# Kernel tuning notes

Measured on AMD Instinct MI355X. Metric: run time of the kernel, lower is better.

## Reference

```python
import jax, jax.numpy as jnp
import numpy as np

N_NODES = 8192
EMBED = 64
N_NEURONS = [512, 256, 128]
ACTION_SIZE = 8
BATCH = 4096


def setup_inputs() -> dict:
    key = jax.random.key(0)
    ks = jax.random.split(key, 16)
    in_size = 2 * N_NODES + 2 * EMBED

    def u(k, shape, bound):
        return jax.random.uniform(k, shape, jnp.float32, -bound, bound)

    stdv1 = 1.0 / np.sqrt(N_NEURONS[0])
    stdv2 = 1.0 / np.sqrt(EMBED)
    return {
        "state": jax.random.uniform(ks[0], (N_NODES, N_NODES), jnp.float32),
        "start": jax.random.randint(ks[1], (BATCH,), 0, N_NODES),
        "end": jax.random.randint(ks[2], (BATCH,), 0, N_NODES),
        # GCN layer params
        "gw1": u(ks[3], (1, N_NEURONS[0]), stdv1),
        "gb1": u(ks[4], (N_NEURONS[0],), stdv1),
        "gw2": u(ks[5], (N_NEURONS[0], EMBED), stdv2),
        "gb2": u(ks[6], (EMBED,), stdv2),
        # dense head params (xavier-ish)
        "fw1": u(ks[7], (in_size, N_NEURONS[0]), np.sqrt(6.0 / (in_size + N_NEURONS[0]))),
        "fb1": jnp.zeros((N_NEURONS[0],), jnp.float32),
        "fw2": u(ks[8], (N_NEURONS[0], N_NEURONS[1]), np.sqrt(6.0 / (N_NEURONS[0] + N_NEURONS[1]))),
        "fb2": jnp.zeros((N_NEURONS[1],), jnp.float32),
        "fw3": u(ks[9], (N_NEURONS[1], N_NEURONS[2]), np.sqrt(6.0 / (N_NEURONS[1] + N_NEURONS[2]))),
        "fb3": jnp.zeros((N_NEURONS[2],), jnp.float32),
        "fw4": u(ks[10], (N_NEURONS[2], ACTION_SIZE), np.sqrt(6.0 / (N_NEURONS[2] + ACTION_SIZE))),
        "fb4": jnp.zeros((ACTION_SIZE,), jnp.float32),
    }


def reference(state, start, end, gw1, gb1, gw2, gb2,
              fw1, fb1, fw2, fb2, fw3, fb3, fw4, fb4):
    # x = diag(state) as [N, 1] node features
    x = jnp.diagonal(state)[:, None]
    # adj = state with zeroed diagonal, detached (no grad through adj)
    adj = jax.lax.stop_gradient(jnp.fill_diagonal(state, 0.0, inplace=False))
    # GCN layer 1: relu(adj @ (x @ W) + b); dropout is identity in eval mode
    h = jax.nn.relu(adj @ (x @ gw1) + gb1)              # [N, 512]
    # GCN layer 2
    h = jax.nn.relu(adj @ (h @ gw2) + gb2)              # [N, 64]
    h = jax.nn.log_softmax(h, axis=1)                   # [N, 64]
    # gather node features and embeddings for each (start, end) edge
    edge_features = jnp.concatenate(
        [state[start], state[end], h[start], h[end]], axis=1)  # [B, 2N+2E]
    y = jax.nn.relu(edge_features @ fw1 + fb1)
    y = jax.nn.relu(y @ fw2 + fb2)                      # d1 dropout: identity (eval)
    y = jax.nn.relu(y @ fw3 + fb3)
    action_q = jax.nn.relu(y @ fw4 + fb4)               # [B, action_size]
    return action_q
```

## Files before the change

### kernel.cpp

```cpp
#include <hip/hip_runtime.h>
#include <hip/hip_bf16.h>
#include <math.h>

#define NN 8192
#define EMB 64
#define H1D 512
#define NB 4096

typedef __bf16 bf16x8 __attribute__((ext_vector_type(8)));
typedef float f32x4 __attribute__((ext_vector_type(4)));
typedef unsigned short u16x8 __attribute__((ext_vector_type(8)));
typedef unsigned short u16x4 __attribute__((ext_vector_type(4)));

__device__ __forceinline__ unsigned short f2bf(float f) {
    return __bfloat16_as_ushort(__float2bfloat16(f));
}

__device__ __forceinline__ void gload16(const void* g, void* l) {
    __builtin_amdgcn_global_load_lds(
        (const __attribute__((address_space(1))) void*)g,
        (__attribute__((address_space(3))) void*)l, 16, 0, 0);
}

__global__ void k_diag(const float* __restrict__ state, float* __restrict__ diag) {
    int i = blockIdx.x * blockDim.x + threadIdx.x;
    if (i < NN) diag[i] = state[(size_t)i * NN + i];
}

__global__ __launch_bounds__(256) void k_convert(const float* __restrict__ state,
                                                 const float* __restrict__ diag,
                                                 unsigned short* __restrict__ stateb,
                                                 float* __restrict__ s) {
    int row = blockIdx.x;
    int tid = threadIdx.x;
    const float4* st4 = (const float4*)(state + (size_t)row * NN);
    const float4* dg4 = (const float4*)diag;
    unsigned short* drow = stateb + (size_t)row * NN;
    float acc = 0.f;
#pragma unroll
    for (int t = 0; t < 8; ++t) {
        int f = t * 256 + tid;
        float4 a = st4[f], d = dg4[f];
        acc += a.x * d.x + a.y * d.y + a.z * d.z + a.w * d.w;
        u16x4 o;
        o[0] = f2bf(a.x); o[1] = f2bf(a.y); o[2] = f2bf(a.z); o[3] = f2bf(a.w);
        *(u16x4*)&drow[f * 4] = o;
    }
#pragma unroll
    for (int m = 32; m >= 1; m >>= 1) acc += __shfl_xor(acc, m);
    __shared__ float red[4];
    if ((tid & 63) == 0) red[tid >> 6] = acc;
    __syncthreads();
    if (tid == 0) {
        float tot = red[0] + red[1] + red[2] + red[3];
        float d = diag[row];
        s[row] = tot - d * d;
    }
}

__global__ __launch_bounds__(256) void k_tr_fw1(const float* __restrict__ fw1,
                                                unsigned short* __restrict__ fw1t) {
    __shared__ float t[64][65];
    int kb = blockIdx.x * 64, nb = blockIdx.y * 64;
    int tid = threadIdx.x;
#pragma unroll
    for (int i = 0; i < 4; ++i) {
        int lin = i * 256 + tid;
        int r = lin >> 4, c4 = (lin & 15) << 2;
        float4 v = *(const float4*)&fw1[(size_t)(kb + r) * 512 + nb + c4];
        t[r][c4] = v.x; t[r][c4 + 1] = v.y; t[r][c4 + 2] = v.z; t[r][c4 + 3] = v.w;
    }
    __syncthreads();
#pragma unroll
    for (int i = 0; i < 4; ++i) {
        int lin = i * 256 + tid;
        int n = lin >> 4, k4 = (lin & 15) << 2;
        u16x4 o;
        o[0] = f2bf(t[k4 + 0][n]); o[1] = f2bf(t[k4 + 1][n]);
        o[2] = f2bf(t[k4 + 2][n]); o[3] = f2bf(t[k4 + 3][n]);
        *(u16x4*)&fw1t[(size_t)(nb + n) * 16512 + kb + k4] = o;
    }
}

__global__ __launch_bounds__(256) void k_tr_q(const float* __restrict__ q,
                                              unsigned short* __restrict__ qbT) {
    __shared__ float t[64][65];
    int kb = blockIdx.x * 64;
    int tid = threadIdx.x;
#pragma unroll
    for (int i = 0; i < 4; ++i) {
        int lin = i * 256 + tid;
        int r = lin >> 4, c4 = (lin & 15) << 2;
        float4 v = *(const float4*)&q[(size_t)(kb + r) * 64 + c4];
        t[r][c4] = v.x; t[r][c4 + 1] = v.y; t[r][c4 + 2] = v.z; t[r][c4 + 3] = v.w;
    }
    __syncthreads();
#pragma unroll
    for (int i = 0; i < 4; ++i) {
        int lin = i * 256 + tid;
        int c = lin >> 4, k4 = (lin & 15) << 2;
        u16x4 o;
        o[0] = f2bf(t[k4 + 0][c]); o[1] = f2bf(t[k4 + 1][c]);
        o[2] = f2bf(t[k4 + 2][c]); o[3] = f2bf(t[k4 + 3][c]);
        *(u16x4*)&qbT[(size_t)c * 8192 + kb + k4] = o;
    }
}

__global__ __launch_bounds__(256) void k_rowdot(const float* __restrict__ state,
                                                const float* __restrict__ diag,
                                                float* __restrict__ s) {
    int row = blockIdx.x;
    int tid = threadIdx.x;
    const float4* st4 = (const float4*)(state + (size_t)row * NN);
    const float4* dg4 = (const float4*)diag;
    float acc = 0.f;
#pragma unroll
    for (int t = 0; t < 8; ++t) {
        int f = t * 256 + tid;
        float4 a = st4[f], d = dg4[f];
        acc += a.x * d.x + a.y * d.y + a.z * d.z + a.w * d.w;
    }
#pragma unroll
    for (int m = 32; m >= 1; m >>= 1) acc += __shfl_xor(acc, m);
    __shared__ float red[4];
    if ((tid & 63) == 0) red[tid >> 6] = acc;
    __syncthreads();
    if (tid == 0) {
        float tot = red[0] + red[1] + red[2] + red[3];
        float d = diag[row];
        s[row] = tot - d * d;
    }
}

__global__ __launch_bounds__(256) void k_q(const float* __restrict__ s,
                                           const float* __restrict__ gw1,
                                           const float* __restrict__ gb1,
                                           const float* __restrict__ gw2,
                                           float* __restrict__ q) {
    int tid = threadIdx.x;
    int c = tid & 63;
    int row = blockIdx.x * 4 + (tid >> 6);
    float sv = s[row];
    float acc = 0.f;
    for (int j = 0; j < H1D; ++j) {
        float hv = fmaxf(fmaf(sv, gw1[j], gb1[j]), 0.f);
        acc = fmaf(hv, gw2[j * EMB + c], acc);
    }
    q[row * EMB + c] = acc;
}


__global__ __launch_bounds__(256) void k_gcn2_mfma_b(const unsigned short* __restrict__ stateb,
                                                     const unsigned short* __restrict__ qbT,
                                                     float* __restrict__ partg) {
    __shared__ __align__(16) unsigned short Asm[2][64 * 64];
    __shared__ __align__(16) unsigned short Bsm[2][64 * 64];
    const int tid = threadIdx.x;
    const int l = tid & 63, wv = tid >> 6;
    const int rbase = blockIdx.x * 64;
    const int kbase0 = blockIdx.y * 1024;

    const unsigned short* aP[2]; const unsigned short* bP[2]; int lb[2];
#pragma unroll
    for (int i = 0; i < 2; ++i) {
        int slot = i * 256 + tid;
        int r = slot >> 3, cg = slot & 7;
        aP[i] = stateb + (size_t)(rbase + r) * NN + kbase0 + ((cg ^ (r & 7)) << 3);
        bP[i] = qbT + (size_t)r * 8192 + kbase0 + ((cg ^ (r & 7)) << 3);
        lb[i] = (i * 256 + wv * 64) * 8;
    }

    f32x4 acc[4] = {};
    const int fr = l & 15, fq = l >> 4;

#pragma unroll
    for (int i = 0; i < 2; ++i) {
        gload16(aP[i], &Asm[0][lb[i]]);
        gload16(bP[i], &Bsm[0][lb[i]]);
    }
    __syncthreads();

    int buf = 0;
    for (int kt = 0; kt < 16; ++kt) {
        if (kt < 15) {
#pragma unroll
            for (int i = 0; i < 2; ++i) {
                gload16(aP[i] + (kt + 1) * 64, &Asm[buf ^ 1][lb[i]]);
                gload16(bP[i] + (kt + 1) * 64, &Bsm[buf ^ 1][lb[i]]);
            }
        }
#pragma unroll
        for (int kh = 0; kh < 2; ++kh) {
            int ch = kh * 4 + fq;
            int row = wv * 16 + fr;
            bf16x8 aF = *(const bf16x8*)&Asm[buf][row * 64 + ((ch ^ (row & 7)) << 3)];
            bf16x8 bF[4];
#pragma unroll
            for (int n = 0; n < 4; ++n) {
                int col = n * 16 + fr;
                bF[n] = *(const bf16x8*)&Bsm[buf][col * 64 + ((ch ^ (col & 7)) << 3)];
            }
#pragma unroll
            for (int n = 0; n < 4; ++n)
                acc[n] = __builtin_amdgcn_mfma_f32_16x16x32_bf16(aF, bF[n], acc[n], 0, 0, 0);
        }
        __syncthreads();
        buf ^= 1;
    }

    float* dst = partg + (size_t)blockIdx.y * (NN * EMB);
#pragma unroll
    for (int n = 0; n < 4; ++n) {
        int row0 = rbase + wv * 16 + fq * 4;
        int col = n * 16 + fr;
#pragma unroll
        for (int j = 0; j < 4; ++j)
            dst[(size_t)(row0 + j) * EMB + col] = acc[n][j];
    }
}

__global__ __launch_bounds__(256) void k_gcn2_combine_b(const float* __restrict__ partg,
                                                        const float* __restrict__ diag,
                                                        const float* __restrict__ q,
                                                        const float* __restrict__ gb2,
                                                        unsigned short* __restrict__ hb) {
    int tid = threadIdx.x;
    int c = tid & 63;
    int row = blockIdx.x * 4 + (tid >> 6);
    int idx = row * EMB + c;
    float v = gb2[c] - diag[row] * q[idx];
#pragma unroll
    for (int p = 0; p < 8; ++p) v += partg[(size_t)p * NN * EMB + idx];
    v = fmaxf(v, 0.f);
    float mx = v;
#pragma unroll
    for (int m = 32; m >= 1; m >>= 1) mx = fmaxf(mx, __shfl_xor(mx, m));
    float e = expf(v - mx);
    float sum = e;
#pragma unroll
    for (int m = 32; m >= 1; m >>= 1) sum += __shfl_xor(sum, m);
    hb[idx] = f2bf(v - mx - logf(sum));
}

__global__ __launch_bounds__(256) void k_head1_mfma_b(
    const unsigned short* __restrict__ stateb, const unsigned short* __restrict__ hb,
    const int* __restrict__ start, const int* __restrict__ end,
    const unsigned short* __restrict__ fw1t, float* __restrict__ parth) {
    __shared__ __align__(16) unsigned short Asm[2][64 * 64];
    __shared__ __align__(16) unsigned short Bsm[2][128 * 64];
    __shared__ int ridx[64];
    const int tid = threadIdx.x;
    const int l = tid & 63, wv = tid >> 6;
    const int rbase = blockIdx.x * 64, cbase = blockIdx.y * 128;
    const int ks = blockIdx.z, side = ks >> 1, half = ks & 1;
    if (tid < 64) ridx[tid] = (side ? end : start)[rbase + tid];
    __syncthreads();

    const unsigned short* aS[2]; const unsigned short* aH[2]; int alb[2];
#pragma unroll
    for (int i = 0; i < 2; ++i) {
        int slot = i * 256 + tid;
        int r = slot >> 3, cg = slot & 7;
        int swz = (cg ^ (r & 7)) << 3;
        int gi = ridx[r];
        aS[i] = stateb + (size_t)gi * NN + half * 4096 + swz;
        aH[i] = hb + gi * EMB + swz;
        alb[i] = (i * 256 + wv * 64) * 8;
    }
    const unsigned short* bP[4]; int blb[4];
#pragma unroll
    for (int i = 0; i < 4; ++i) {
        int slot = i * 256 + tid;
        int n = slot >> 3, cg = slot & 7;
        bP[i] = fw1t + (size_t)(cbase + n) * 16512 + ((cg ^ (n & 7)) << 3);
        blb[i] = (i * 256 + wv * 64) * 8;
    }
    const int kB0 = side * 8192 + half * 4096;
    const int kBtail = 16384 + side * 64;
    const int nsteps = 64 + half;

#pragma unroll
    for (int i = 0; i < 2; ++i) gload16(aS[i], &Asm[0][alb[i]]);
#pragma unroll
    for (int i = 0; i < 4; ++i) gload16(bP[i] + kB0, &Bsm[0][blb[i]]);
    __syncthreads();

    f32x4 acc[2][4] = {};
    const int wm = wv >> 1, wn = wv & 1;
    const int fr = l & 15, fq = l >> 4;

    int buf = 0;
    for (int kt = 0; kt < nsteps; ++kt) {
        int nxt = kt + 1;
        if (nxt < nsteps) {
            if (nxt < 64) {
#pragma unroll
                for (int i = 0; i < 2; ++i) gload16(aS[i] + nxt * 64, &Asm[buf ^ 1][alb[i]]);
#pragma unroll
                for (int i = 0; i < 4; ++i) gload16(bP[i] + kB0 + nxt * 64, &Bsm[buf ^ 1][blb[i]]);
            } else {
#pragma unroll
                for (int i = 0; i < 2; ++i) gload16(aH[i], &Asm[buf ^ 1][alb[i]]);
#pragma unroll
                for (int i = 0; i < 4; ++i) gload16(bP[i] + kBtail, &Bsm[buf ^ 1][blb[i]]);
            }
        }
#pragma unroll
        for (int kh = 0; kh < 2; ++kh) {
            int ch = kh * 4 + fq;
            bf16x8 aF[2], bF[4];
#pragma unroll
            for (int m = 0; m < 2; ++m) {
                int row = wm * 32 + m * 16 + fr;
                aF[m] = *(const bf16x8*)&Asm[buf][row * 64 + ((ch ^ (row & 7)) << 3)];
            }
#pragma unroll
            for (int n = 0; n < 4; ++n) {
                int nl = wn * 64 + n * 16 + fr;
                bF[n] = *(const bf16x8*)&Bsm[buf][nl * 64 + ((ch ^ (nl & 7)) << 3)];
            }
#pragma unroll
            for (int m = 0; m < 2; ++m)
#pragma unroll
                for (int n = 0; n < 4; ++n)
                    acc[m][n] = __builtin_amdgcn_mfma_f32_16x16x32_bf16(
                        aF[m], bF[n], acc[m][n], 0, 0, 0);
        }
        __syncthreads();
        buf ^= 1;
    }

    float* dst = parth + (size_t)ks * (NB * H1D);
#pragma unroll
    for (int m = 0; m < 2; ++m) {
        int row0 = rbase + wm * 32 + m * 16 + fq * 4;
#pragma unroll
        for (int n = 0; n < 4; ++n) {
            int col = cbase + wn * 64 + n * 16 + fr;
#pragma unroll
            for (int j = 0; j < 4; ++j)
                dst[(size_t)(row0 + j) * H1D + col] = acc[m][n][j];
        }
    }
}

__global__ void k_head1_fin4(const float* __restrict__ parth, const float* __restrict__ fb1,
                             float* __restrict__ y1) {
    int i = blockIdx.x * blockDim.x + threadIdx.x;
    const size_t S = (size_t)NB * H1D;
    float4 a = *(const float4*)&parth[(size_t)i * 4];
    float4 b = *(const float4*)&parth[S + (size_t)i * 4];
    float4 c = *(const float4*)&parth[2 * S + (size_t)i * 4];
    float4 d = *(const float4*)&parth[3 * S + (size_t)i * 4];
    float4 bias = *(const float4*)&fb1[(i * 4) & 511];
    float4 o;
    o.x = fmaxf(a.x + b.x + c.x + d.x + bias.x, 0.f);
    o.y = fmaxf(a.y + b.y + c.y + d.y + bias.y, 0.f);
    o.z = fmaxf(a.z + b.z + c.z + d.z + bias.z, 0.f);
    o.w = fmaxf(a.w + b.w + c.w + d.w + bias.w, 0.f);
    *(float4*)&y1[(size_t)i * 4] = o;
}


__global__ __launch_bounds__(256) void k_gcn2_mfma(const float* __restrict__ state,
                                                   const unsigned short* __restrict__ qbT,
                                                   float* __restrict__ partg) {
    __shared__ __align__(16) unsigned short Asm[2][64 * 64];
    __shared__ __align__(16) unsigned short Bsm[2][64 * 64];
    const int tid = threadIdx.x;
    const int l = tid & 63, wv = tid >> 6;
    const int rbase = blockIdx.x * 64;
    const int kbase0 = blockIdx.y * 1024;

    const float* aptr[2]; int awr[2];
#pragma unroll
    for (int i = 0; i < 2; ++i) {
        int slot = i * 256 + tid;
        int r = slot >> 3, cg = slot & 7;
        aptr[i] = state + (size_t)(rbase + r) * NN + kbase0 + cg * 8;
        awr[i] = r * 64 + ((cg ^ (r & 7)) << 3);
    }
    const unsigned short* bptr[2]; int bbase[2];
#pragma unroll
    for (int i = 0; i < 2; ++i) {
        int c = i * 32 + wv * 8 + (l >> 3);
        int cg = l & 7;
        bptr[i] = qbT + (size_t)c * 8192 + kbase0 + ((cg ^ (c & 7)) << 3);
        bbase[i] = i * 2048 + wv * 512;
    }

    f32x4 acc[4] = {};
    const int fr = l & 15, fq = l >> 4;
    float4 va[2][2];

#pragma unroll
    for (int i = 0; i < 2; ++i) {
        va[i][0] = *(const float4*)aptr[i];
        va[i][1] = *(const float4*)(aptr[i] + 4);
    }
#pragma unroll
    for (int i = 0; i < 2; ++i) {
        u16x8 o;
        o[0] = f2bf(va[i][0].x); o[1] = f2bf(va[i][0].y); o[2] = f2bf(va[i][0].z); o[3] = f2bf(va[i][0].w);
        o[4] = f2bf(va[i][1].x); o[5] = f2bf(va[i][1].y); o[6] = f2bf(va[i][1].z); o[7] = f2bf(va[i][1].w);
        *(u16x8*)&Asm[0][awr[i]] = o;
        gload16(bptr[i], &Bsm[0][bbase[i]]);
    }
    __syncthreads();

    int buf = 0;
    for (int kt = 0; kt < 16; ++kt) {
        if (kt < 15) {
#pragma unroll
            for (int i = 0; i < 2; ++i) {
                gload16(bptr[i] + (kt + 1) * 64, &Bsm[buf ^ 1][bbase[i]]);
                va[i][0] = *(const float4*)(aptr[i] + (kt + 1) * 64);
                va[i][1] = *(const float4*)(aptr[i] + (kt + 1) * 64 + 4);
            }
        }
#pragma unroll
        for (int kh = 0; kh < 2; ++kh) {
            int ch = kh * 4 + fq;
            int row = wv * 16 + fr;
            bf16x8 aF = *(const bf16x8*)&Asm[buf][row * 64 + ((ch ^ (row & 7)) << 3)];
            bf16x8 bF[4];
#pragma unroll
            for (int n = 0; n < 4; ++n) {
                int col = n * 16 + fr;
                bF[n] = *(const bf16x8*)&Bsm[buf][col * 64 + ((ch ^ (col & 7)) << 3)];
            }
#pragma unroll
            for (int n = 0; n < 4; ++n)
                acc[n] = __builtin_amdgcn_mfma_f32_16x16x32_bf16(aF, bF[n], acc[n], 0, 0, 0);
        }
        if (kt < 15) {
#pragma unroll
            for (int i = 0; i < 2; ++i) {
                u16x8 o;
                o[0] = f2bf(va[i][0].x); o[1] = f2bf(va[i][0].y); o[2] = f2bf(va[i][0].z); o[3] = f2bf(va[i][0].w);
                o[4] = f2bf(va[i][1].x); o[5] = f2bf(va[i][1].y); o[6] = f2bf(va[i][1].z); o[7] = f2bf(va[i][1].w);
                *(u16x8*)&Asm[buf ^ 1][awr[i]] = o;
            }
        }
        __syncthreads();
        buf ^= 1;
    }

    float* dst = partg + (size_t)blockIdx.y * (NN * EMB);
#pragma unroll
    for (int n = 0; n < 4; ++n) {
        int row0 = rbase + wv * 16 + fq * 4;
        int col = n * 16 + fr;
#pragma unroll
        for (int j = 0; j < 4; ++j)
            dst[(size_t)(row0 + j) * EMB + col] = acc[n][j];
    }
}

__global__ __launch_bounds__(256) void k_gcn2_combine(const float* __restrict__ partg,
                                                      const float* __restrict__ diag,
                                                      const float* __restrict__ q,
                                                      const float* __restrict__ gb2,
                                                      float* __restrict__ h) {
    int tid = threadIdx.x;
    int c = tid & 63;
    int row = blockIdx.x * 4 + (tid >> 6);
    int idx = row * EMB + c;
    float v = gb2[c] - diag[row] * q[idx];
#pragma unroll
    for (int p = 0; p < 8; ++p) v += partg[(size_t)p * NN * EMB + idx];
    v = fmaxf(v, 0.f);
    float mx = v;
#pragma unroll
    for (int m = 32; m >= 1; m >>= 1) mx = fmaxf(mx, __shfl_xor(mx, m));
    float e = expf(v - mx);
    float sum = e;
#pragma unroll
    for (int m = 32; m >= 1; m >>= 1) sum += __shfl_xor(sum, m);
    h[idx] = v - mx - logf(sum);
}

__global__ __launch_bounds__(256) void k_head1_mfma(
    const float* __restrict__ state, const float* __restrict__ h,
    const int* __restrict__ start, const int* __restrict__ end,
    const unsigned short* __restrict__ fw1t, float* __restrict__ part) {
    __shared__ __align__(16) unsigned short Asm[2][64 * 64];
    __shared__ __align__(16) unsigned short Bsm[2][128 * 64];
    __shared__ int ridx[64];
    const int tid = threadIdx.x;
    const int l = tid & 63, wv = tid >> 6;
    const int rbase = blockIdx.x * 64, cbase = blockIdx.y * 128;
    const int ks = blockIdx.z;
    if (tid < 64) ridx[tid] = (ks ? end : start)[rbase + tid];
    __syncthreads();

    const float* aptr[2]; const float* hptr[2]; int awr[2];
#pragma unroll
    for (int i = 0; i < 2; ++i) {
        int slot = i * 256 + tid;
        int r = slot >> 3, cg = slot & 7;
        int gi = ridx[r];
        aptr[i] = state + (size_t)gi * NN + cg * 8;
        hptr[i] = h + gi * EMB + cg * 8;
        awr[i] = r * 64 + ((cg ^ (r & 7)) << 3);
    }
    const unsigned short* bptr[4]; int bbase[4];
#pragma unroll
    for (int i = 0; i < 4; ++i) {
        int n = i * 32 + wv * 8 + (l >> 3);
        int cg = l & 7;
        bptr[i] = fw1t + (size_t)(cbase + n) * 16512 + ((cg ^ (n & 7)) << 3);
        bbase[i] = i * 2048 + wv * 512;
    }

    f32x4 acc[2][4] = {};
    const int wm = wv >> 1, wn = wv & 1;
    const int fr = l & 15, fq = l >> 4;
    float4 va[2][2];

#pragma unroll
    for (int i = 0; i < 2; ++i) {
        va[i][0] = *(const float4*)aptr[i];
        va[i][1] = *(const float4*)(aptr[i] + 4);
    }
#pragma unroll
    for (int i = 0; i < 2; ++i) {
        u16x8 o;
        o[0] = f2bf(va[i][0].x); o[1] = f2bf(va[i][0].y); o[2] = f2bf(va[i][0].z); o[3] = f2bf(va[i][0].w);
        o[4] = f2bf(va[i][1].x); o[5] = f2bf(va[i][1].y); o[6] = f2bf(va[i][1].z); o[7] = f2bf(va[i][1].w);
        *(u16x8*)&Asm[0][awr[i]] = o;
    }
#pragma unroll
    for (int i = 0; i < 4; ++i) gload16(bptr[i] + ks * 8192, &Bsm[0][bbase[i]]);
    __syncthreads();

    int buf = 0;
    for (int kt = 0; kt < 129; ++kt) {
        if (kt < 128) {
            int nxt = kt + 1;
            int kB = (nxt < 128) ? (ks * 8192 + nxt * 64) : (16384 + ks * 64);
#pragma unroll
            for (int i = 0; i < 4; ++i) gload16(bptr[i] + kB, &Bsm[buf ^ 1][bbase[i]]);
#pragma unroll
            for (int i = 0; i < 2; ++i) {
                const float* src = (nxt < 128) ? (aptr[i] + nxt * 64) : hptr[i];
                va[i][0] = *(const float4*)src;
                va[i][1] = *(const float4*)(src + 4);
            }
        }
#pragma unroll
        for (int kh = 0; kh < 2; ++kh) {
            int ch = kh * 4 + fq;
            bf16x8 aF[2], bF[4];
#pragma unroll
            for (int m = 0; m < 2; ++m) {
                int row = wm * 32 + m * 16 + fr;
                aF[m] = *(const bf16x8*)&Asm[buf][row * 64 + ((ch ^ (row & 7)) << 3)];
            }
#pragma unroll
            for (int n = 0; n < 4; ++n) {
                int nl = wn * 64 + n * 16 + fr;
                bF[n] = *(const bf16x8*)&Bsm[buf][nl * 64 + ((ch ^ (nl & 7)) << 3)];
            }
#pragma unroll
            for (int m = 0; m < 2; ++m)
#pragma unroll
                for (int n = 0; n < 4; ++n)
                    acc[m][n] = __builtin_amdgcn_mfma_f32_16x16x32_bf16(
                        aF[m], bF[n], acc[m][n], 0, 0, 0);
        }
        if (kt < 128) {
#pragma unroll
            for (int i = 0; i < 2; ++i) {
                u16x8 o;
                o[0] = f2bf(va[i][0].x); o[1] = f2bf(va[i][0].y); o[2] = f2bf(va[i][0].z); o[3] = f2bf(va[i][0].w);
                o[4] = f2bf(va[i][1].x); o[5] = f2bf(va[i][1].y); o[6] = f2bf(va[i][1].z); o[7] = f2bf(va[i][1].w);
                *(u16x8*)&Asm[buf ^ 1][awr[i]] = o;
            }
        }
        __syncthreads();
        buf ^= 1;
    }

    float* dst = part + (size_t)ks * (NB * H1D);
#pragma unroll
    for (int m = 0; m < 2; ++m) {
        int row0 = rbase + wm * 32 + m * 16 + fq * 4;
#pragma unroll
        for (int n = 0; n < 4; ++n) {
            int col = cbase + wn * 64 + n * 16 + fr;
#pragma unroll
            for (int j = 0; j < 4; ++j)
                dst[(size_t)(row0 + j) * H1D + col] = acc[m][n][j];
        }
    }
}

__global__ void k_head1_fin(const float* __restrict__ part, const float* __restrict__ fb1,
                            float* __restrict__ y1) {
    int i = blockIdx.x * blockDim.x + threadIdx.x;
    float4 a = *(const float4*)&part[(size_t)i * 4];
    float4 b = *(const float4*)&part[(size_t)NB * H1D + (size_t)i * 4];
    float4 bias = *(const float4*)&fb1[(i * 4) & 511];
    float4 o;
    o.x = fmaxf(a.x + b.x + bias.x, 0.f);
    o.y = fmaxf(a.y + b.y + bias.y, 0.f);
    o.z = fmaxf(a.z + b.z + bias.z, 0.f);
    o.w = fmaxf(a.w + b.w + bias.w, 0.f);
    *(float4*)&y1[(size_t)i * 4] = o;
}

#define GEMM_INNER(AsM, BsM)                                          \
    _Pragma("unroll")                                                 \
    for (int k4 = 0; k4 < 64; k4 += 4) {                              \
        float av[4][4], bv[4][4];                                     \
        _Pragma("unroll")                                             \
        for (int i = 0; i < 4; ++i)                                   \
            *(float4*)av[i] = *(const float4*)&AsM[4 * row_t + i][k4];\
        _Pragma("unroll")                                             \
        for (int t = 0; t < 4; ++t)                                   \
            *(float4*)bv[t] = *(const float4*)&BsM[k4 + t][4 * col_t];\
        _Pragma("unroll")                                             \
        for (int i = 0; i < 4; ++i) {                                 \
            _Pragma("unroll")                                         \
            for (int t = 0; t < 4; ++t) {                             \
                _Pragma("unroll")                                     \
                for (int j = 0; j < 4; ++j)                           \
                    acc[i][j] = fmaf(av[i][t], bv[t][j], acc[i][j]);  \
            }                                                         \
        }                                                             \
    }

__global__ __launch_bounds__(256) void k_gemm_relu(const float* __restrict__ A,
                                                   const float* __restrict__ W,
                                                   const float* __restrict__ bias,
                                                   float* __restrict__ C,
                                                   int M, int N, int K) {
    __shared__ __align__(16) float As[64][68];
    __shared__ __align__(16) float Bs[64][68];
    int tid = threadIdx.x;
    int rbase = blockIdx.x * 64;
    int cbase = blockIdx.y * 64;
    int row_t = tid >> 4, col_t = tid & 15;
    float acc[4][4] = {};
    for (int kt = 0; kt < K / 64; ++kt) {
        int kbase = kt * 64;
#pragma unroll
        for (int l = 0; l < 4; ++l) {
            int lin = l * 256 + tid;
            int r = lin >> 4, k4 = (lin & 15) << 2;
            float4 v = *(const float4*)&A[(size_t)(rbase + r) * K + kbase + k4];
            As[r][k4 + 0] = v.x; As[r][k4 + 1] = v.y; As[r][k4 + 2] = v.z; As[r][k4 + 3] = v.w;
            float4 w = *(const float4*)&W[(size_t)(kbase + r) * N + cbase + k4];
            Bs[r][k4 + 0] = w.x; Bs[r][k4 + 1] = w.y; Bs[r][k4 + 2] = w.z; Bs[r][k4 + 3] = w.w;
        }
        __syncthreads();
        GEMM_INNER(As, Bs)
        __syncthreads();
    }
#pragma unroll
    for (int i = 0; i < 4; ++i) {
        int row = rbase + 4 * row_t + i;
        int col = cbase + 4 * col_t;
        float4 v;
        v.x = fmaxf(acc[i][0] + bias[col + 0], 0.f);
        v.y = fmaxf(acc[i][1] + bias[col + 1], 0.f);
        v.z = fmaxf(acc[i][2] + bias[col + 2], 0.f);
        v.w = fmaxf(acc[i][3] + bias[col + 3], 0.f);
        *(float4*)&C[(size_t)row * N + col] = v;
    }
}

__global__ void k_head4(const float* __restrict__ y3, const float* __restrict__ fw4,
                        const float* __restrict__ fb4, float* __restrict__ out) {
    int tid = blockIdx.x * blockDim.x + threadIdx.x;
    int b = tid >> 3, j = tid & 7;
    float acc = fb4[j];
    for (int k = 0; k < 128; ++k)
        acc = fmaf(y3[b * 128 + k], fw4[k * 8 + j], acc);
    out[tid] = fmaxf(acc, 0.f);
}

extern "C" void kernel_launch(void* const* d_in, const int* in_sizes, int n_in,
                              void* d_out, int out_size, void* d_ws, size_t ws_size,
                              hipStream_t stream) {
    const float* state = (const float*)d_in[0];
    const int* start   = (const int*)d_in[1];
    const int* end     = (const int*)d_in[2];
    const float* gw1   = (const float*)d_in[3];
    const float* gb1   = (const float*)d_in[4];
    const float* gw2   = (const float*)d_in[5];
    const float* gb2   = (const float*)d_in[6];
    const float* fw1   = (const float*)d_in[7];
    const float* fb1   = (const float*)d_in[8];
    const float* fw2   = (const float*)d_in[9];
    const float* fb2   = (const float*)d_in[10];
    const float* fw3   = (const float*)d_in[11];
    const float* fb3   = (const float*)d_in[12];
    const float* fw4   = (const float*)d_in[13];
    const float* fb4   = (const float*)d_in[14];
    float* out = (float*)d_out;
    float* ws = (float*)d_ws;

    const size_t NEED_BIG = 51429376ull * 4ull;
    const size_t NEED_FB  = 9748480ull * 4ull;

    if (ws_size >= NEED_BIG) {
        float* diag = ws;
        float* s    = ws + 8192;
        float* q    = ws + 16384;
        unsigned short* qbT = (unsigned short*)(ws + 540672);
        unsigned short* hb  = (unsigned short*)(ws + 802816);
        float* partg = ws + 1064960;
        unsigned short* fw1t = (unsigned short*)(ws + 5259264);
        unsigned short* stateb = (unsigned short*)(ws + 9486336);
        float* parth = ws + 43040768;
        float* y1   = ws + 5259264;
        float* y2   = ws + 16384;
        float* y3   = ws + 7356416;

        k_diag<<<32, 256, 0, stream>>>(state, diag);
        k_convert<<<8192, 256, 0, stream>>>(state, diag, stateb, s);
        k_tr_fw1<<<dim3(258, 8), 256, 0, stream>>>(fw1, fw1t);
        k_q<<<2048, 256, 0, stream>>>(s, gw1, gb1, gw2, q);
        k_tr_q<<<128, 256, 0, stream>>>(q, qbT);
        k_gcn2_mfma_b<<<dim3(128, 8), 256, 0, stream>>>(stateb, qbT, partg);
        k_gcn2_combine_b<<<2048, 256, 0, stream>>>(partg, diag, q, gb2, hb);
        k_head1_mfma_b<<<dim3(64, 4, 4), 256, 0, stream>>>(stateb, hb, start, end, fw1t, parth);
        k_head1_fin4<<<2048, 256, 0, stream>>>(parth, fb1, y1);
        k_gemm_relu<<<dim3(64, 4), 256, 0, stream>>>(y1, fw2, fb2, y2, NB, 256, 512);
        k_gemm_relu<<<dim3(64, 2), 256, 0, stream>>>(y2, fw3, fb3, y3, NB, 128, 256);
        k_head4<<<128, 256, 0, stream>>>(y3, fw4, fb4, out);
        return;
    }

    if (ws_size < NEED_FB) return;

    float* diag = ws;
    float* s    = ws + 8192;
    float* q    = ws + 16384;
    unsigned short* qbT = (unsigned short*)(ws + 540672);
    float* h    = ws + 802816;
    float* partg = ws + 1327104;
    unsigned short* fw1t = (unsigned short*)(ws + 5521408);
    float* parth = ws + 1327104;
    float* y1   = ws + 5521408;
    float* y2   = ws + 16384;
    float* y3   = ws + 7618560;

    k_diag<<<32, 256, 0, stream>>>(state, diag);
    k_tr_fw1<<<dim3(258, 8), 256, 0, stream>>>(fw1, fw1t);
    k_rowdot<<<8192, 256, 0, stream>>>(state, diag, s);
    k_q<<<2048, 256, 0, stream>>>(s, gw1, gb1, gw2, q);
    k_tr_q<<<128, 256, 0, stream>>>(q, qbT);
    k_gcn2_mfma<<<dim3(128, 8), 256, 0, stream>>>(state, qbT, partg);
    k_gcn2_combine<<<2048, 256, 0, stream>>>(partg, diag, q, gb2, h);
    k_head1_mfma<<<dim3(64, 4, 2), 256, 0, stream>>>(state, h, start, end, fw1t, parth);
    k_head1_fin<<<2048, 256, 0, stream>>>(parth, fb1, y1);
    k_gemm_relu<<<dim3(64, 4), 256, 0, stream>>>(y1, fw2, fb2, y2, NB, 256, 512);
    k_gemm_relu<<<dim3(64, 2), 256, 0, stream>>>(y2, fw3, fb3, y3, NB, 128, 256);
    k_head4<<<128, 256, 0, stream>>>(y3, fw4, fb4, out);
}
```

Baseline: 330.0 us.

## Enlarge head1 GEMM tile to 128x128, drop double buffering, unroll k_q accumulators

The head1 MFMA kernel now computes a 128x128 output tile per block instead of 64x128. This doubles reuse of the fw1 B-tile and halves the grid to 512 blocks. Double-buffered LDS is replaced by a single buffer with load, sync, compute, sync, so global loads no longer overlap with MFMA work, and the tighter loop may cost latency. Separately, k_q uses four independent accumulators to break the serial FMA dependency chain.

```diff
diff --git a/kernel.cpp b/kernel.cpp
--- a/kernel.cpp
+++ b/kernel.cpp
@@ -141,12 +141,18 @@
     int c = tid & 63;
     int row = blockIdx.x * 4 + (tid >> 6);
     float sv = s[row];
-    float acc = 0.f;
-    for (int j = 0; j < H1D; ++j) {
-        float hv = fmaxf(fmaf(sv, gw1[j], gb1[j]), 0.f);
-        acc = fmaf(hv, gw2[j * EMB + c], acc);
-    }
-    q[row * EMB + c] = acc;
+    float a0 = 0.f, a1 = 0.f, a2 = 0.f, a3 = 0.f;
+    for (int j = 0; j < H1D; j += 4) {
+        float h0 = fmaxf(fmaf(sv, gw1[j + 0], gb1[j + 0]), 0.f);
+        float h1 = fmaxf(fmaf(sv, gw1[j + 1], gb1[j + 1]), 0.f);
+        float h2 = fmaxf(fmaf(sv, gw1[j + 2], gb1[j + 2]), 0.f);
+        float h3 = fmaxf(fmaf(sv, gw1[j + 3], gb1[j + 3]), 0.f);
+        a0 = fmaf(h0, gw2[(j + 0) * EMB + c], a0);
+        a1 = fmaf(h1, gw2[(j + 1) * EMB + c], a1);
+        a2 = fmaf(h2, gw2[(j + 2) * EMB + c], a2);
+        a3 = fmaf(h3, gw2[(j + 3) * EMB + c], a3);
+    }
+    q[row * EMB + c] = (a0 + a1) + (a2 + a3);
 }
 
 
@@ -246,94 +252,82 @@
     const unsigned short* __restrict__ stateb, const unsigned short* __restrict__ hb,
     const int* __restrict__ start, const int* __restrict__ end,
     const unsigned short* __restrict__ fw1t, float* __restrict__ parth) {
-    __shared__ __align__(16) unsigned short Asm[2][64 * 64];
-    __shared__ __align__(16) unsigned short Bsm[2][128 * 64];
-    __shared__ int ridx[64];
+    __shared__ __align__(16) unsigned short Asm[128 * 64];
+    __shared__ __align__(16) unsigned short Bsm[128 * 64];
+    __shared__ int ridx[128];
     const int tid = threadIdx.x;
     const int l = tid & 63, wv = tid >> 6;
-    const int rbase = blockIdx.x * 64, cbase = blockIdx.y * 128;
+    const int rbase = blockIdx.x * 128, cbase = blockIdx.y * 128;
     const int ks = blockIdx.z, side = ks >> 1, half = ks & 1;
-    if (tid < 64) ridx[tid] = (side ? end : start)[rbase + tid];
-    __syncthreads();
-
-    const unsigned short* aS[2]; const unsigned short* aH[2]; int alb[2];
-#pragma unroll
-    for (int i = 0; i < 2; ++i) {
+    if (tid < 128) ridx[tid] = (side ? end : start)[rbase + tid];
+    __syncthreads();
+
+    const unsigned short* aS[4]; const unsigned short* aH[4];
+    const unsigned short* bP[4];
+    unsigned short* aL[4]; unsigned short* bL[4];
+#pragma unroll
+    for (int i = 0; i < 4; ++i) {
         int slot = i * 256 + tid;
         int r = slot >> 3, cg = slot & 7;
         int swz = (cg ^ (r & 7)) << 3;
         int gi = ridx[r];
         aS[i] = stateb + (size_t)gi * NN + half * 4096 + swz;
         aH[i] = hb + gi * EMB + swz;
-        alb[i] = (i * 256 + wv * 64) * 8;
-    }
-    const unsigned short* bP[4]; int blb[4];
-#pragma unroll
-    for (int i = 0; i < 4; ++i) {
-        int slot = i * 256 + tid;
-        int n = slot >> 3, cg = slot & 7;
-        bP[i] = fw1t + (size_t)(cbase + n) * 16512 + ((cg ^ (n & 7)) << 3);
-        blb[i] = (i * 256 + wv * 64) * 8;
+        bP[i] = fw1t + (size_t)(cbase + r) * 16512 + swz;
+        aL[i] = &Asm[slot * 8];
+        bL[i] = &Bsm[slot * 8];
     }
     const int kB0 = side * 8192 + half * 4096;
     const int kBtail = 16384 + side * 64;
     const int nsteps = 64 + half;
 
-#pragma unroll
-    for (int i = 0; i < 2; ++i) gload16(aS[i], &Asm[0][alb[i]]);
-#pragma unroll
-    for (int i = 0; i < 4; ++i) gload16(bP[i] + kB0, &Bsm[0][blb[i]]);
-    __syncthreads();
-
-    f32x4 acc[2][4] = {};
+    f32x4 acc[4][4] = {};
     const int wm = wv >> 1, wn = wv & 1;
     const int fr = l & 15, fq = l >> 4;
 
-    int buf = 0;
     for (int kt = 0; kt < nsteps; ++kt) {
-        int nxt = kt + 1;
-        if (nxt < nsteps) {
-            if (nxt < 64) {
-#pragma unroll
-                for (int i = 0; i < 2; ++i) gload16(aS[i] + nxt * 64, &Asm[buf ^ 1][alb[i]]);
-#pragma unroll
-                for (int i = 0; i < 4; ++i) gload16(bP[i] + kB0 + nxt * 64, &Bsm[buf ^ 1][blb[i]]);
-            } else {
-#pragma unroll
-                for (int i = 0; i < 2; ++i) gload16(aH[i], &Asm[buf ^ 1][alb[i]]);
-#pragma unroll
-                for (int i = 0; i < 4; ++i) gload16(bP[i] + kBtail, &Bsm[buf ^ 1][blb[i]]);
-            }
-        }
+        if (kt < 64) {
+#pragma unroll
+            for (int i = 0; i < 4; ++i) {
+                gload16(aS[i] + kt * 64, aL[i]);
+                gload16(bP[i] + kB0 + kt * 64, bL[i]);
+            }
+        } else {
+#pragma unroll
+            for (int i = 0; i < 4; ++i) {
+                gload16(aH[i], aL[i]);
+                gload16(bP[i] + kBtail, bL[i]);
+            }
+        }
+        __syncthreads();
 #pragma unroll
         for (int kh = 0; kh < 2; ++kh) {
             int ch = kh * 4 + fq;
-            bf16x8 aF[2], bF[4];
-#pragma unroll
-            for (int m = 0; m < 2; ++m) {
-                int row = wm * 32 + m * 16 + fr;
-                aF[m] = *(const bf16x8*)&Asm[buf][row * 64 + ((ch ^ (row & 7)) << 3)];
+            bf16x8 aF[4], bF[4];
+#pragma unroll
+            for (int m = 0; m < 4; ++m) {
+                int row = wm * 64 + m * 16 + fr;
+                aF[m] = *(const bf16x8*)&Asm[row * 64 + ((ch ^ (row & 7)) << 3)];
             }
 #pragma unroll
             for (int n = 0; n < 4; ++n) {
                 int nl = wn * 64 + n * 16 + fr;
-                bF[n] = *(const bf16x8*)&Bsm[buf][nl * 64 + ((ch ^ (nl & 7)) << 3)];
-            }
-#pragma unroll
-            for (int m = 0; m < 2; ++m)
+                bF[n] = *(const bf16x8*)&Bsm[nl * 64 + ((ch ^ (nl & 7)) << 3)];
+            }
+#pragma unroll
+            for (int m = 0; m < 4; ++m)
 #pragma unroll
                 for (int n = 0; n < 4; ++n)
                     acc[m][n] = __builtin_amdgcn_mfma_f32_16x16x32_bf16(
                         aF[m], bF[n], acc[m][n], 0, 0, 0);
         }
         __syncthreads();
-        buf ^= 1;
     }
 
     float* dst = parth + (size_t)ks * (NB * H1D);
 #pragma unroll
-    for (int m = 0; m < 2; ++m) {
-        int row0 = rbase + wm * 32 + m * 16 + fq * 4;
+    for (int m = 0; m < 4; ++m) {
+        int row0 = rbase + wm * 64 + m * 16 + fq * 4;
 #pragma unroll
         for (int n = 0; n < 4; ++n) {
             int col = cbase + wn * 64 + n * 16 + fr;
@@ -726,7 +720,7 @@
         k_tr_q<<<128, 256, 0, stream>>>(q, qbT);
         k_gcn2_mfma_b<<<dim3(128, 8), 256, 0, stream>>>(stateb, qbT, partg);
         k_gcn2_combine_b<<<2048, 256, 0, stream>>>(partg, diag, q, gb2, hb);
-        k_head1_mfma_b<<<dim3(64, 4, 4), 256, 0, stream>>>(stateb, hb, start, end, fw1t, parth);
+        k_head1_mfma_b<<<dim3(32, 4, 4), 256, 0, stream>>>(stateb, hb, start, end, fw1t, parth);
         k_head1_fin4<<<2048, 256, 0, stream>>>(parth, fb1, y1);
         k_gemm_relu<<<dim3(64, 4), 256, 0, stream>>>(y1, fw2, fb2, y2, NB, 256, 512);
         k_gemm_relu<<<dim3(64, 2), 256, 0, stream>>>(y2, fw3, fb3, y3, NB, 128, 256);
```

Result: faster. 293.9 us (-10.9%).
